# Kernel optimization log

Hardware: AMD Instinct MI355X
Metric: run time of the kernel (lower is better)

The kernel has to match this reference:

```python
import jax, jax.numpy as jnp
import numpy as np

T, B, D = 512, 64, 1024


def setup_inputs() -> dict:
    key = jax.random.key(0)
    k1, k2, k3, k4, k5 = jax.random.split(key, 5)
    s = 1.0 / np.sqrt(D)  # torch RNNCell init scale
    return {
        "x": jax.random.normal(k1, (T, B, D), dtype=jnp.float32),
        "W_ih": jax.random.normal(k2, (D, D), dtype=jnp.float32) * s,
        "W_hh": jax.random.normal(k3, (D, D), dtype=jnp.float32) * s,
        "b_ih": jax.random.normal(k4, (D,), dtype=jnp.float32) * s,
        "b_hh": jax.random.normal(k5, (D,), dtype=jnp.float32) * s,
    }


def reference(x, W_ih, W_hh, b_ih, b_hh):
    """CustomRNN forward: sequential Elman cell over time-major input.

    x: [T, B, D]; returns (output [T, B, D], final hidden [B, D]).
    """
    # Precompute the input projection for all timesteps in one big GEMM
    # (same math as per-step x_t @ W_ih^T + b_ih, just batched).
    xproj = jnp.einsum("tbd,hd->tbh", x, W_ih) + b_ih  # [T, B, D]

    def step(h, xp_t):
        h_new = jnp.tanh(xp_t + h @ W_hh.T + b_hh)  # [B, D]
        return h_new, h_new

    h0 = jnp.zeros((x.shape[1], W_hh.shape[0]), dtype=x.dtype)
    h_final, output = jax.lax.scan(step, h0, xproj)
    return output, h_final
```

## Files before the change

kernel.cpp:

```cpp
#include <hip/hip_runtime.h>
#include <hip/hip_bf16.h>

#define T_LEN 512
#define B_SZ  64
#define D_SZ  1024

typedef __attribute__((ext_vector_type(8))) short  short8;
typedef __attribute__((ext_vector_type(4))) float  f32x4;
typedef __attribute__((ext_vector_type(4))) unsigned short ushort4v;
typedef __attribute__((ext_vector_type(4))) unsigned int   uint4v;

__device__ __forceinline__ float bf2f(unsigned short u) {
    unsigned int x = ((unsigned int)u) << 16;
    return __uint_as_float(x);
}
__device__ __forceinline__ unsigned short f2bf(float f) {
    unsigned int x = __float_as_uint(f);
    unsigned int r = x + 0x7FFFu + ((x >> 16) & 1u);
    return (unsigned short)(r >> 16);
}
__device__ __forceinline__ void split2p(float f, unsigned short* hi, unsigned short* lo) {
    unsigned short h = f2bf(f);
    *hi = h;
    *lo = f2bf(f - bf2f(h));
}
__device__ __forceinline__ float fast_tanh(float x) {
    float xx = fminf(fmaxf(x, -20.0f), 20.0f);
    float e2 = __expf(2.0f * xx);
    return __fdividef(e2 - 1.0f, e2 + 1.0f);
}

#define CNT_STRIDE 64

__global__ void init_kernel(int* slot) {
    int i = threadIdx.x;
    if (i < 8 * CNT_STRIDE) slot[i] = 0;
}

#define BM 128
#define BN 128
#define BK 32
#define ASTR (BK + 8)

__global__ __launch_bounds__(256) void xproj_kernel(
    const float* __restrict__ x, const float* __restrict__ Wih,
    const float* __restrict__ bih, float* __restrict__ xp)
{
    __shared__ unsigned short Ah[BM][ASTR];
    __shared__ unsigned short Al[BM][ASTR];
    __shared__ unsigned short Bh[BN][ASTR];
    __shared__ unsigned short Bl[BN][ASTR];

    const int nblk = D_SZ / BN;
    const int bm = blockIdx.x / nblk;
    const int bn = blockIdx.x % nblk;
    const int m0 = bm * BM, n0 = bn * BN;
    const int tid  = threadIdx.x;
    const int lane = tid & 63, wave = tid >> 6;
    const int wm = wave >> 1, wn = wave & 1;

    f32x4 acc[4][4];
#pragma unroll
    for (int i = 0; i < 4; i++)
#pragma unroll
        for (int j = 0; j < 4; j++) acc[i][j] = (f32x4)0.0f;

    const int ar = lane & 15;
    const int kb = (lane >> 4) << 3;

    for (int k0 = 0; k0 < D_SZ; k0 += BK) {
#pragma unroll
        for (int i = 0; i < 4; i++) {
            int f4  = tid + i * 256;
            int row = f4 >> 3;
            int c4  = (f4 & 7) << 2;
            f32x4 va = *reinterpret_cast<const f32x4*>(x   + (size_t)(m0 + row) * D_SZ + k0 + c4);
            f32x4 vb = *reinterpret_cast<const f32x4*>(Wih + (size_t)(n0 + row) * D_SZ + k0 + c4);
            ushort4v pah, pal, pbh, pbl;
#pragma unroll
            for (int e = 0; e < 4; e++) {
                unsigned short h_, l_;
                split2p(va[e], &h_, &l_); pah[e] = h_; pal[e] = l_;
                split2p(vb[e], &h_, &l_); pbh[e] = h_; pbl[e] = l_;
            }
            *reinterpret_cast<ushort4v*>(&Ah[row][c4]) = pah;
            *reinterpret_cast<ushort4v*>(&Al[row][c4]) = pal;
            *reinterpret_cast<ushort4v*>(&Bh[row][c4]) = pbh;
            *reinterpret_cast<ushort4v*>(&Bl[row][c4]) = pbl;
        }
        __syncthreads();

        short8 ah[4], al[4], bh[4], bl[4];
#pragma unroll
        for (int mi = 0; mi < 4; mi++) {
            ah[mi] = *reinterpret_cast<const short8*>(&Ah[wm * 64 + mi * 16 + ar][kb]);
            al[mi] = *reinterpret_cast<const short8*>(&Al[wm * 64 + mi * 16 + ar][kb]);
        }
#pragma unroll
        for (int ni = 0; ni < 4; ni++) {
            bh[ni] = *reinterpret_cast<const short8*>(&Bh[wn * 64 + ni * 16 + ar][kb]);
            bl[ni] = *reinterpret_cast<const short8*>(&Bl[wn * 64 + ni * 16 + ar][kb]);
        }
#pragma unroll
        for (int mi = 0; mi < 4; mi++)
#pragma unroll
            for (int ni = 0; ni < 4; ni++) {
                acc[mi][ni] = __builtin_amdgcn_mfma_f32_16x16x32_bf16(ah[mi], bh[ni], acc[mi][ni], 0, 0, 0);
                acc[mi][ni] = __builtin_amdgcn_mfma_f32_16x16x32_bf16(al[mi], bh[ni], acc[mi][ni], 0, 0, 0);
                acc[mi][ni] = __builtin_amdgcn_mfma_f32_16x16x32_bf16(ah[mi], bl[ni], acc[mi][ni], 0, 0, 0);
            }
        __syncthreads();
    }

    const int r0 = (lane >> 4) * 4;
    const int cl = lane & 15;
#pragma unroll
    for (int mi = 0; mi < 4; mi++) {
#pragma unroll
        for (int ni = 0; ni < 4; ni++) {
            int col = n0 + wn * 64 + ni * 16 + cl;
            float bias = bih[col];
            size_t base = (size_t)(m0 + wm * 64 + mi * 16 + r0) * D_SZ + col;
#pragma unroll
            for (int r = 0; r < 4; r++)
                xp[base + (size_t)r * D_SZ] = acc[mi][ni][r] + bias;
        }
    }
}

#define MR 8
#define NC 32
#define HSTR (D_SZ + 8)
#define WSTR 520

__global__ __launch_bounds__(128, 1) void rnn_kernel(
    const float* __restrict__ xp, const float* __restrict__ Whh,
    const float* __restrict__ bhh, float* __restrict__ out,
    unsigned int* hbuf, int* slot)
{
    __shared__ unsigned short Hh[16][HSTR];
    __shared__ unsigned short Hl[16][HSTR];
    __shared__ unsigned short Wlo[2][16][WSTR];

    const int wg = blockIdx.x;
    const int b  = wg & 7;
    const int c  = wg >> 3;
    const int tid  = threadIdx.x;
    const int lane = tid & 63, wave = tid >> 6;

    const int cl   = lane & 15;
    const int hi4  = lane >> 4;
    const int kb   = hi4 << 3;
    const int colg = c * NC + wave * 16 + cl;
    const float bias = bhh[colg];
    const int rloc = hi4 * 4;
    const bool active = (hi4 < 2);

    int* tslot = slot + b * CNT_STRIDE;
    const int myslot = c * 2 + wave;

    short8 wh[32], wl_r[16];
    {
        const float* wrow = Whh + (size_t)colg * D_SZ;
#pragma unroll
        for (int kk = 0; kk < 32; kk++) {
            f32x4 v0 = *reinterpret_cast<const f32x4*>(wrow + kk * 32 + kb);
            f32x4 v1 = *reinterpret_cast<const f32x4*>(wrow + kk * 32 + kb + 4);
            short8 sh, sl;
#pragma unroll
            for (int e = 0; e < 4; e++) {
                unsigned short h_, l_;
                split2p(v0[e], &h_, &l_); sh[e] = (short)h_; sl[e] = (short)l_;
                split2p(v1[e], &h_, &l_); sh[4 + e] = (short)h_; sl[4 + e] = (short)l_;
            }
            wh[kk] = sh;
            if (kk < 16) wl_r[kk] = sl;
            else *reinterpret_cast<short8*>(&Wlo[wave][cl][(kk - 16) * 32 + kb]) = sl;
        }
    }
    for (int i = tid; i < 16 * HSTR; i += 128) {
        (&Hh[0][0])[i] = 0;
        (&Hl[0][0])[i] = 0;
    }
    __syncthreads();

    for (int t = 0; t < T_LEN; t++) {
        float xv[4];
        const float* xpt = xp + ((size_t)t * B_SZ + b * MR) * D_SZ;
        if (active) {
#pragma unroll
            for (int r = 0; r < 4; r++)
                xv[r] = xpt[(size_t)(rloc + r) * D_SZ + colg];
        }

        uint4v vv[16];
        if (t > 0) {
            for (int tries = 0; tries < 400000; ++tries) {
                int v = __hip_atomic_load(tslot + lane, __ATOMIC_RELAXED, __HIP_MEMORY_SCOPE_AGENT);
                if (__all(v >= t)) break;
            }

            asm volatile("s_waitcnt vmcnt(0)" ::: "memory");

            const uint4v* hsrc16 = reinterpret_cast<const uint4v*>(
                hbuf + ((size_t)(t & 1) * B_SZ + b * MR) * D_SZ);
#pragma unroll
            for (int s = 0; s < 16; s++) {
                int i = (s < 8) ? (2 * s) : (2 * (s - 8) + 1);
                asm volatile("global_load_dwordx4 %0, %1, off sc0 sc1"
                             : "=v"(vv[s]) : "v"(hsrc16 + tid + i * 128) : "memory");
            }
            asm volatile("s_waitcnt vmcnt(8)" ::: "memory");
            __builtin_amdgcn_sched_barrier(0);
#pragma unroll
            for (int s = 0; s < 8; s++) {
                int j   = tid + (2 * s) * 128;
                int row = j >> 8;
                int c4  = (j & 255) << 2;
                ushort4v hh, hl;
#pragma unroll
                for (int e = 0; e < 4; e++) {
                    unsigned int u = vv[s][e];
                    hh[e] = (unsigned short)(u & 0xFFFFu);
                    hl[e] = (unsigned short)(u >> 16);
                }
                *reinterpret_cast<ushort4v*>(&Hh[row][c4]) = hh;
                *reinterpret_cast<ushort4v*>(&Hl[row][c4]) = hl;
            }
            __syncthreads();
        }

        f32x4 a0 = (f32x4)0.0f, a1 = (f32x4)0.0f, a2 = (f32x4)0.0f;
#pragma unroll
        for (int kk = 0; kk < 16; kk++) {
            short8 ah  = *reinterpret_cast<const short8*>(&Hh[cl][kk * 32 + kb]);
            short8 alo = *reinterpret_cast<const short8*>(&Hl[cl][kk * 32 + kb]);
            a0 = __builtin_amdgcn_mfma_f32_16x16x32_bf16(ah,  wh[kk],   a0, 0, 0, 0);
            a1 = __builtin_amdgcn_mfma_f32_16x16x32_bf16(alo, wh[kk],   a1, 0, 0, 0);
            a2 = __builtin_amdgcn_mfma_f32_16x16x32_bf16(ah,  wl_r[kk], a2, 0, 0, 0);
        }

        if (t > 0) {
            asm volatile("s_waitcnt vmcnt(0)" ::: "memory");
            __builtin_amdgcn_sched_barrier(0);
#pragma unroll
            for (int s = 8; s < 16; s++) {
                int j   = tid + (2 * (s - 8) + 1) * 128;
                int row = j >> 8;
                int c4  = (j & 255) << 2;
                ushort4v hh, hl;
#pragma unroll
                for (int e = 0; e < 4; e++) {
                    unsigned int u = vv[s][e];
                    hh[e] = (unsigned short)(u & 0xFFFFu);
                    hl[e] = (unsigned short)(u >> 16);
                }
                *reinterpret_cast<ushort4v*>(&Hh[row][c4]) = hh;
                *reinterpret_cast<ushort4v*>(&Hl[row][c4]) = hl;
            }
            __syncthreads();
        }

#pragma unroll
        for (int kk = 16; kk < 32; kk++) {
            short8 ah  = *reinterpret_cast<const short8*>(&Hh[cl][kk * 32 + kb]);
            short8 alo = *reinterpret_cast<const short8*>(&Hl[cl][kk * 32 + kb]);
            short8 wlv = *reinterpret_cast<const short8*>(&Wlo[wave][cl][(kk - 16) * 32 + kb]);
            a0 = __builtin_amdgcn_mfma_f32_16x16x32_bf16(ah,  wh[kk], a0, 0, 0, 0);
            a1 = __builtin_amdgcn_mfma_f32_16x16x32_bf16(alo, wh[kk], a1, 0, 0, 0);
            a2 = __builtin_amdgcn_mfma_f32_16x16x32_bf16(ah,  wlv,    a2, 0, 0, 0);
        }

        float hval[4];
        if (active) {
            unsigned int* hdst = hbuf + ((size_t)((t + 1) & 1) * B_SZ + b * MR) * D_SZ;
#pragma unroll
            for (int r = 0; r < 4; r++) {
                int row = rloc + r;
                float pre = (a0[r] + a1[r] + a2[r]) + xv[r] + bias;
                float h = fast_tanh(pre);
                hval[r] = h;
                unsigned short hh_, ll_;
                split2p(h, &hh_, &ll_);
                unsigned int packed = (unsigned int)hh_ | ((unsigned int)ll_ << 16);
                __hip_atomic_store(&hdst[(size_t)row * D_SZ + colg], packed,
                                   __ATOMIC_RELAXED, __HIP_MEMORY_SCOPE_AGENT);
            }
        }
        asm volatile("s_waitcnt vmcnt(0)" ::: "memory");
        if (lane == 0)
            __hip_atomic_store(tslot + myslot, t + 1, __ATOMIC_RELAXED, __HIP_MEMORY_SCOPE_AGENT);

        if (active) {
            float* outt = out + ((size_t)t * B_SZ + b * MR) * D_SZ;
#pragma unroll
            for (int r = 0; r < 4; r++) {
                int row = rloc + r;
                outt[(size_t)row * D_SZ + colg] = hval[r];
                if (t == T_LEN - 1)
                    out[(size_t)T_LEN * B_SZ * D_SZ + (size_t)(b * MR + row) * D_SZ + colg] = hval[r];
            }
        }
    }
}

extern "C" void kernel_launch(void* const* d_in, const int* in_sizes, int n_in,
                              void* d_out, int out_size, void* d_ws, size_t ws_size,
                              hipStream_t stream)
{
    const float* x   = (const float*)d_in[0];
    const float* Wih = (const float*)d_in[1];
    const float* Whh = (const float*)d_in[2];
    const float* bih = (const float*)d_in[3];
    const float* bhh = (const float*)d_in[4];
    float* out = (float*)d_out;

    char* ws = (char*)d_ws;
    float*        xp   = (float*)ws;
    unsigned int* hbuf = (unsigned int*)(ws + 134217728);
    int*          slot = (int*)(ws + 134217728 + 524288);

    init_kernel<<<dim3(1), dim3(512), 0, stream>>>(slot);
    xproj_kernel<<<dim3(2048), dim3(256), 0, stream>>>(x, Wih, bih, xp);
    rnn_kernel<<<dim3(256), dim3(128), 0, stream>>>(xp, Whh, bhh, out, hbuf, slot);
}
```

Baseline: 2.475 ms.

## Use 4-wave workgroups with 64 columns each and drop split h-load pipelining

Each recurrent workgroup now has 4 waves and covers 64 hidden columns instead of 32, which halves the grid to 128 blocks and the number of participants in each batch group's barrier. Each thread loads half as much of the previous hidden state, and the two-phase load/convert that overlapped the second half with the first 16 MFMA steps is replaced by a single load, wait and LDS store. This cuts the per-step cross-workgroup synchronization fan-in and the redundant hidden-state reads. In exchange it loses the overlap of global loads with compute. The slot polling still reads 64 lanes, so it relies on the counter layout matching the new slot indexing.

```diff
diff --git a/kernel.cpp b/kernel.cpp
--- a/kernel.cpp
+++ b/kernel.cpp
@@ -129,18 +129,18 @@
 }
 
 #define MR 8
-#define NC 32
+#define NC 64
 #define HSTR (D_SZ + 8)
 #define WSTR 520
 
-__global__ __launch_bounds__(128, 1) void rnn_kernel(
+__global__ __launch_bounds__(256, 1) void rnn_kernel(
     const float* __restrict__ xp, const float* __restrict__ Whh,
     const float* __restrict__ bhh, float* __restrict__ out,
     unsigned int* hbuf, int* slot)
 {
     __shared__ unsigned short Hh[16][HSTR];
     __shared__ unsigned short Hl[16][HSTR];
-    __shared__ unsigned short Wlo[2][16][WSTR];
+    __shared__ unsigned short Wlo[4][16][WSTR];
 
     const int wg = blockIdx.x;
     const int b  = wg & 7;
@@ -157,7 +157,7 @@
     const bool active = (hi4 < 2);
 
     int* tslot = slot + b * CNT_STRIDE;
-    const int myslot = c * 2 + wave;
+    const int myslot = c * 4 + wave;
 
     short8 wh[32], wl_r[16];
     {
@@ -178,7 +178,7 @@
             else *reinterpret_cast<short8*>(&Wlo[wave][cl][(kk - 16) * 32 + kb]) = sl;
         }
     }
-    for (int i = tid; i < 16 * HSTR; i += 128) {
+    for (int i = tid; i < 16 * HSTR; i += 256) {
         (&Hh[0][0])[i] = 0;
         (&Hl[0][0])[i] = 0;
     }
@@ -193,34 +193,30 @@
                 xv[r] = xpt[(size_t)(rloc + r) * D_SZ + colg];
         }
 
-        uint4v vv[16];
         if (t > 0) {
             for (int tries = 0; tries < 400000; ++tries) {
                 int v = __hip_atomic_load(tslot + lane, __ATOMIC_RELAXED, __HIP_MEMORY_SCOPE_AGENT);
                 if (__all(v >= t)) break;
             }
 
-            asm volatile("s_waitcnt vmcnt(0)" ::: "memory");
-
             const uint4v* hsrc16 = reinterpret_cast<const uint4v*>(
                 hbuf + ((size_t)(t & 1) * B_SZ + b * MR) * D_SZ);
-#pragma unroll
-            for (int s = 0; s < 16; s++) {
-                int i = (s < 8) ? (2 * s) : (2 * (s - 8) + 1);
+            uint4v vv[8];
+#pragma unroll
+            for (int i = 0; i < 8; i++)
                 asm volatile("global_load_dwordx4 %0, %1, off sc0 sc1"
-                             : "=v"(vv[s]) : "v"(hsrc16 + tid + i * 128) : "memory");
-            }
-            asm volatile("s_waitcnt vmcnt(8)" ::: "memory");
+                             : "=v"(vv[i]) : "v"(hsrc16 + tid + i * 256) : "memory");
+            asm volatile("s_waitcnt vmcnt(0)" ::: "memory");
             __builtin_amdgcn_sched_barrier(0);
 #pragma unroll
-            for (int s = 0; s < 8; s++) {
-                int j   = tid + (2 * s) * 128;
+            for (int i = 0; i < 8; i++) {
+                int j   = tid + i * 256;
                 int row = j >> 8;
                 int c4  = (j & 255) << 2;
                 ushort4v hh, hl;
 #pragma unroll
                 for (int e = 0; e < 4; e++) {
-                    unsigned int u = vv[s][e];
+                    unsigned int u = vv[i][e];
                     hh[e] = (unsigned short)(u & 0xFFFFu);
                     hl[e] = (unsigned short)(u >> 16);
                 }
@@ -239,28 +235,6 @@
             a1 = __builtin_amdgcn_mfma_f32_16x16x32_bf16(alo, wh[kk],   a1, 0, 0, 0);
             a2 = __builtin_amdgcn_mfma_f32_16x16x32_bf16(ah,  wl_r[kk], a2, 0, 0, 0);
         }
-
-        if (t > 0) {
-            asm volatile("s_waitcnt vmcnt(0)" ::: "memory");
-            __builtin_amdgcn_sched_barrier(0);
-#pragma unroll
-            for (int s = 8; s < 16; s++) {
-                int j   = tid + (2 * (s - 8) + 1) * 128;
-                int row = j >> 8;
-                int c4  = (j & 255) << 2;
-                ushort4v hh, hl;
-#pragma unroll
-                for (int e = 0; e < 4; e++) {
-                    unsigned int u = vv[s][e];
-                    hh[e] = (unsigned short)(u & 0xFFFFu);
-                    hl[e] = (unsigned short)(u >> 16);
-                }
-                *reinterpret_cast<ushort4v*>(&Hh[row][c4]) = hh;
-                *reinterpret_cast<ushort4v*>(&Hl[row][c4]) = hl;
-            }
-            __syncthreads();
-        }
-
 #pragma unroll
         for (int kk = 16; kk < 32; kk++) {
             short8 ah  = *reinterpret_cast<const short8*>(&Hh[cl][kk * 32 + kb]);
@@ -322,5 +296,5 @@
 
     init_kernel<<<dim3(1), dim3(512), 0, stream>>>(slot);
     xproj_kernel<<<dim3(2048), dim3(256), 0, stream>>>(x, Wih, bih, xp);
-    rnn_kernel<<<dim3(256), dim3(128), 0, stream>>>(xp, Whh, bhh, out, hbuf, slot);
-}
+    rnn_kernel<<<dim3(128), dim3(256), 0, stream>>>(xp, Whh, bhh, out, hbuf, slot);
+}
```

Result: faster. 2.298 ms (-7.1%).
